# Optimization experiments

Hardware: AMD Instinct MI355X
Metric: run time of the kernel (lower is better)

Reference implementation:

```python
import jax, jax.numpy as jnp
import numpy as np

N = 50000          # nodes
E = 1_600_000      # edges (avg degree 32)
D = 128            # in_channels
H = 128            # hidden_channels
B = 4096           # batch_nodes
BETA = 0.5


def setup_inputs() -> dict:
    key = jax.random.key(0)
    ks = jax.random.split(key, 12)
    s = 1.0 / np.sqrt(D)
    inp = {
        "x": jax.random.normal(ks[0], (N, D), jnp.float32),
        "edge_index": jax.random.randint(ks[1], (2, E), 0, N, dtype=jnp.int64),
        "batch_nodes": jax.random.randint(ks[2], (B,), 0, N, dtype=jnp.int64),
        "labels": jax.random.randint(ks[3], (N,), 0, 2, dtype=jnp.int64),
        # GCNConv layer params (weight [in,out], bias [out])
        "W1": jax.random.uniform(ks[4], (D, H), jnp.float32, -s, s),
        "b1": jnp.zeros((H,), jnp.float32),
        "W2": jax.random.uniform(ks[5], (H, H), jnp.float32, -s, s),
        "b2": jnp.zeros((H,), jnp.float32),
        # Bilinear heads: weight [H,H] (out_features=1), scalar bias
        "W_ctx": jax.random.uniform(ks[6], (H, H), jnp.float32, -s, s),
        "b_ctx": jnp.zeros((), jnp.float32),
        "W_loc": jax.random.uniform(ks[7], (H, H), jnp.float32, -s, s),
        "b_loc": jnp.zeros((), jnp.float32),
    }
    return inp


def _gcn_conv(h, W, b, src, dst, n):
    """PyG GCNConv: linear transform, add self-loops, sym-normalized scatter-add."""
    h = h @ W  # [n, out]
    loop = jnp.arange(n, dtype=src.dtype)
    src_f = jnp.concatenate([src, loop])
    dst_f = jnp.concatenate([dst, loop])
    deg = jax.ops.segment_sum(jnp.ones_like(dst_f, dtype=h.dtype), dst_f, num_segments=n)
    dinv = jnp.where(deg > 0, jax.lax.rsqrt(deg), 0.0)
    norm = dinv[src_f] * dinv[dst_f]                      # [E+n]
    msg = h[src_f] * norm[:, None]                        # gather + scale
    out = jax.ops.segment_sum(msg, dst_f, num_segments=n)  # scatter-add
    return out + b


def _bce_logits(z, y):
    # mean(softplus(z) - z*y) == BCEWithLogits
    return jnp.mean(jax.nn.softplus(z) - z * y)


def reference(x, edge_index, batch_nodes, labels, W1, b1, W2, b2, W_ctx, b_ctx, W_loc, b_loc):
    src, dst = edge_index[0], edge_index[1]
    n = x.shape[0]
    layers = [(W1, b1), (W2, b2)]

    # eval mode: dropout is identity
    h = x
    for W, b in layers:
        h = jax.nn.relu(_gcn_conv(h, W, b, src, dst, n))

    gf = h[batch_nodes]                                   # [B, H]
    y = (labels[batch_nodes] == 1).astype(gf.dtype)       # [B]
    pos_cnt = jnp.sum(y)
    neg_cnt = y.shape[0] - pos_cnt
    pos_proto = (y[:, None] * gf).sum(0) / pos_cnt        # [H]

    # context bilinear head: z_i = gf_i^T W_ctx pos_proto + b (neg_sim is dead code in source)
    pos_sim = gf @ (W_ctx @ pos_proto) + b_ctx            # [B]
    ctx_loss = _bce_logits(pos_sim, y)

    # environment view: zero out batch nodes, re-run GCN stack (no dropout in source)
    masked_x = x.at[batch_nodes].set(0.0)
    env_h = masked_x
    for W, b in layers:
        env_h = jax.nn.relu(_gcn_conv(env_h, W, b, src, dst, n))
    env_f = env_h[batch_nodes]                            # [B, H]

    local_sim = jnp.einsum('nd,de,ne->n', env_f, W_loc, gf) + b_loc
    local_loss = _bce_logits(local_sim, 1.0 - y)

    total_loss = BETA * ctx_loss + (1.0 - BETA) * local_loss
    # source's guard: both classes present (true w.h.p. for random labels)
    total_loss = jnp.where((pos_cnt > 0) & (neg_cnt > 0), total_loss, 0.0)
    return gf, total_loss
```

## Files before the change

### kernel.cpp

```cpp
#include <hip/hip_runtime.h>
#include <math.h>

#define HID 128
#define BSH 7
#define BNODES 128
#define CAP 6144
#define NBK 512
#define EPB 4096

typedef _Float16 h2v __attribute__((ext_vector_type(2)));
typedef _Float16 h8v __attribute__((ext_vector_type(8)));
typedef float f4v __attribute__((ext_vector_type(4)));

static inline int ceil_div(int a, int b) { return (a + b - 1) / b; }


__global__ __launch_bounds__(256) void k_setup(const float* __restrict__ W1, const float* __restrict__ W2,
                                               const float* __restrict__ Wl, _Float16* T1, _Float16* T2,
                                               _Float16* Tl, unsigned int* mask, int* bcur,
                                               float* part, float* pcnt_raw, float* lsums, int* donecnt,
                                               int mw, int NB) {
    int b = blockIdx.x;
    int t = threadIdx.x;
    if (b < 192) {
        int which = b >> 6;
        int idx = (b & 63) * 256 + t;
        int k = idx >> 7, c = idx & 127;
        const float* S = (which == 0) ? W1 : ((which == 1) ? W2 : Wl);
        _Float16* D = (which == 0) ? T1 : ((which == 1) ? T2 : Tl);
        D[c * 128 + k] = (_Float16)S[idx];
    } else {
        int i = (b - 192) * 256 + t;
        if (i < mw) mask[i] = 0u;
        if (i < NB) bcur[i] = i * CAP;
        if (b == 192) {
            if (t < 128) part[t] = 0.f;
            else if (t == 128) pcnt_raw[0] = 0.f;
            else if (t < 131) lsums[t - 129] = 0.f;
            else if (t == 131) donecnt[0] = 0;
        }
    }
}


__global__ __launch_bounds__(1024) void k_partA(const int* __restrict__ ei, int* __restrict__ bcur,
                                                unsigned int* __restrict__ ebuf,
                                                const int* __restrict__ batch, unsigned int* mask,
                                                int E, int B, int NB, int NBLKE) {
    if ((int)blockIdx.x >= NBLKE) {
        int i = ((int)blockIdx.x - NBLKE) * 1024 + threadIdx.x;
        if (i < B) { int nd = batch[i]; atomicOr(&mask[nd >> 5], 1u << (nd & 31)); }
        return;
    }
    __shared__ int lcnt[NBK];
    __shared__ int sc[NBK];
    __shared__ int lcur[NBK];
    __shared__ int gbase[NBK];
    __shared__ unsigned int se[EPB];
    int tid = threadIdx.x;
    if (tid < NBK) lcnt[tid] = 0;
    __syncthreads();
    int base = blockIdx.x * EPB;
    unsigned int pk[4];
    int bk[4];
#pragma unroll
    for (int j = 0; j < 4; ++j) {
        int e = base + tid + j * 1024;
        if (e < E) {
            int s = ei[e], d = ei[E + e];
            pk[j] = ((unsigned int)s << 8) | (unsigned int)(d & 127);
            bk[j] = d >> BSH;
            atomicAdd(&lcnt[bk[j]], 1);
        } else bk[j] = -1;
    }
    __syncthreads();
    if (tid < NBK) sc[tid] = lcnt[tid];
    __syncthreads();
    for (int off = 1; off < NBK; off <<= 1) {
        int v = 0;
        if (tid < NBK && tid >= off) v = sc[tid - off];
        __syncthreads();
        if (tid < NBK) sc[tid] += v;
        __syncthreads();
    }
    if (tid < NBK) {
        int cc = lcnt[tid];
        lcur[tid] = sc[tid] - cc;
        gbase[tid] = cc ? atomicAdd(&bcur[tid], cc) : 0;
    }
    __syncthreads();
#pragma unroll
    for (int j = 0; j < 4; ++j) {
        if (bk[j] >= 0) {
            int r = atomicAdd(&lcur[bk[j]], 1);
            se[r] = pk[j];
        }
    }
    __syncthreads();
    int wid = tid >> 6, lane = tid & 63;
    for (int b2 = wid; b2 < NB; b2 += 16) {
        int cc = lcnt[b2];
        int lo = sc[b2] - cc;
        int go = gbase[b2];
        for (int i = lane; i < cc; i += 64) ebuf[go + i] = se[lo + i];
    }
}


__global__ __launch_bounds__(256) void k_csr(const unsigned int* __restrict__ ebuf, const int* __restrict__ bcur,
                                             const unsigned int* __restrict__ mask,
                                             float* __restrict__ sdinv, int* __restrict__ rs,
                                             int* __restrict__ degpk, unsigned int* __restrict__ csr, int N) {
    __shared__ unsigned int se[CAP];
    __shared__ int deg[BNODES];
    __shared__ int fde[BNODES];
    __shared__ int sc[BNODES];
    __shared__ int cu[BNODES];
    __shared__ int cf[BNODES];
    int b = blockIdx.x, t = threadIdx.x;
    if (t < BNODES) { deg[t] = 0; fde[t] = 0; }
    __syncthreads();
    int base = b * CAP;
    int ecnt = bcur[b] - base;
    for (int i = t; i < ecnt; i += 256) {
        unsigned int v = ebuf[base + i];
        int s = v >> 8;
        int fl = (mask[s >> 5] >> (s & 31)) & 1;
        se[i] = ((unsigned int)s << 9) | ((unsigned int)fl << 8) | (v & 255);
        atomicAdd(&deg[v & 255], 1);
        if (fl) atomicAdd(&fde[v & 255], 1);
    }
    __syncthreads();
    int dv = 0, fv = 0, pv = 0;
    if (t < BNODES) {
        dv = deg[t]; fv = fde[t];
        pv = (dv + 7) & ~7;
        sc[t] = pv;
    }
    __syncthreads();
    for (int off = 1; off < BNODES; off <<= 1) {
        int v2 = (t < BNODES && t >= off) ? sc[t - off] : 0;
        __syncthreads();
        if (t < BNODES) sc[t] += v2;
        __syncthreads();
    }
    int node = b * BNODES + t;
    int r0 = 0;
    if (t < BNODES) {
        r0 = base + sc[t] - pv;
        cu[t] = r0;
        cf[t] = r0 + (dv - fv);
        if (node < N) {
            rs[node] = r0;
            degpk[node] = dv | (fv << 16);
            float di = rsqrtf((float)(dv + 1));
            if ((mask[node >> 5] >> (node & 31)) & 1) di = -di;
            sdinv[node] = di;
        }
    }
    __syncthreads();
    for (int i = t; i < ecnt; i += 256) {
        unsigned int v = se[i];
        int d8 = v & 255;
        int p = ((v >> 8) & 1) ? atomicAdd(&cf[d8], 1) : atomicAdd(&cu[d8], 1);
        csr[p] = v >> 9;
    }
    if (t < BNODES && node < N) {
        for (int j = dv; j < pv; ++j) csr[r0 + j] = (unsigned int)N;
    }
}


__global__ __launch_bounds__(256) void k_cast(const float* __restrict__ x, const float* __restrict__ sdinv,
                                              _Float16* __restrict__ xs, _Float16* __restrict__ H, int N) {
    int i = blockIdx.x * 256 + threadIdx.x;
    int nx = N * 16;
    if (i < nx) {
        int node = i >> 4;
        float da = fabsf(sdinv[node]);
        int o = i * 8;
        float4 a = *(const float4*)&x[o];
        float4 b = *(const float4*)&x[o + 4];
        h8v v;
        v[0] = (_Float16)(a.x * da); v[1] = (_Float16)(a.y * da);
        v[2] = (_Float16)(a.z * da); v[3] = (_Float16)(a.w * da);
        v[4] = (_Float16)(b.x * da); v[5] = (_Float16)(b.y * da);
        v[6] = (_Float16)(b.z * da); v[7] = (_Float16)(b.w * da);
        *(h8v*)&xs[o] = v;
    } else if (i < nx + 16) {
        *(h8v*)&xs[(size_t)i * 8] = (h8v){};
    } else if (i < nx + 16 + 32) {
        int j = i - (nx + 16);
        *(h8v*)&H[(size_t)2 * N * HID + j * 8] = (h8v){};
    }
}


__global__ __launch_bounds__(512) void k_layer1(const _Float16* __restrict__ xs, const int* __restrict__ rs,
                                                const int* __restrict__ degpk, const unsigned int* __restrict__ csr,
                                                const float* __restrict__ sdinv, const _Float16* __restrict__ W1T,
                                                const float* __restrict__ bias, _Float16* __restrict__ H, int N) {
    __shared__ __align__(16) _Float16 sWT[128 * 136];
    __shared__ __align__(16) _Float16 sAgg[64 * 136];
    __shared__ float sbias[128];
    __shared__ float sda[32];
    float* sC = (float*)sWT;

    int tid = threadIdx.x;
    int wave = tid >> 6, lane = tid & 63;
    int grp = lane >> 4, rl = lane & 15;

#pragma unroll
    for (int it = 0; it < 4; ++it) {
        int lin = (it * 512 + tid) * 8;
        int c = lin >> 7, k = lin & 127;
        *(h8v*)&sWT[c * 136 + k] = *(const h8v*)&W1T[lin];
    }
    if (tid < 128) sbias[tid] = bias[tid];
    if (tid < 32) {
        int nd = blockIdx.x * 32 + tid;
        sda[tid] = (nd < N) ? fabsf(sdinv[nd]) : 0.f;
    }

    int ch = rl * 8;
    int lg = wave * 4 + grp;
    int row = blockIdx.x * 32 + lg;
    bool ok = row < N;
    int p = 0, deg = 0, fd = 0;
    float sd = 0.f;
    h8v hs = {};
    if (ok) {
        p = rs[row];
        int dp = degpk[row];
        deg = dp & 0xffff; fd = dp >> 16;
        sd = sdinv[row];
        hs = *(const h8v*)&xs[(size_t)row * HID + ch];
    }
    int ud = deg - fd;
    int pd = (deg + 7) & ~7;
    int t1 = max(pd, __shfl_xor(pd, 16));
    int m  = max(t1, __shfl_xor(t1, 32));
    float U[8] = {}, F[8] = {};
    for (int i = 0; i < m; i += 16) {
        int id[16];
#pragma unroll
        for (int k = 0; k < 16; ++k) {
            int raw = (int)csr[p + i + k];
            id[k] = (i + k < pd) ? raw : N;
        }
        h8v h[16];
#pragma unroll
        for (int k = 0; k < 16; ++k) h[k] = *(const h8v*)&xs[(size_t)id[k] * HID + ch];
        h8v s0 = (h[0] + h[1]) + (h[2] + h[3]);
        h8v s1 = (h[4] + h[5]) + (h[6] + h[7]);
        h8v s2 = (h[8] + h[9]) + (h[10] + h[11]);
        h8v s3 = (h[12] + h[13]) + (h[14] + h[15]);
        h8v s  = (s0 + s1) + (s2 + s3);
#pragma unroll
        for (int j = 0; j < 8; ++j) U[j] += (float)s[j];
        if (i + 16 > ud) {
#pragma unroll
            for (int k = 0; k < 16; ++k) {
                if (i + k >= ud && i + k < deg) {
#pragma unroll
                    for (int j = 0; j < 8; ++j) F[j] += (float)h[k][j];
                }
            }
        }
    }
    {
        float da = fabsf(sd);
        float keep = (sd < 0.f) ? 0.f : 1.f;
        h8v lo = {}, hi = {};
        if (ok) {
#pragma unroll
            for (int j = 0; j < 8; ++j) {
                float f = (float)hs[j];
                lo[j] = (_Float16)(da * (U[j] + f));
                hi[j] = (_Float16)(da * (U[j] - F[j] + keep * f));
            }
        }
        *(h8v*)&sAgg[(2 * lg) * 136 + ch] = lo;
        *(h8v*)&sAgg[(2 * lg + 1) * 136 + ch] = hi;
    }
    __syncthreads();

    int g = lane >> 4;
    int rowtile = (wave & 3) * 16;
    int colbase = (wave >> 2) * 64;
    f4v acc[4];
#pragma unroll
    for (int cc = 0; cc < 4; ++cc) acc[cc] = (f4v){0.f, 0.f, 0.f, 0.f};
#pragma unroll
    for (int kb = 0; kb < 4; ++kb) {
        int k0 = kb * 32 + g * 8;
        h8v av = *(const h8v*)&sAgg[(rowtile + rl) * 136 + k0];
#pragma unroll
        for (int cc = 0; cc < 4; ++cc) {
            h8v bv = *(const h8v*)&sWT[(colbase + cc * 16 + rl) * 136 + k0];
            acc[cc] = __builtin_amdgcn_mfma_f32_16x16x32_f16(bv, av, acc[cc], 0, 0, 0);
        }
    }
    __syncthreads();

    int lrow = rowtile + rl;
    float dsc = sda[lrow >> 1];
#pragma unroll
    for (int cc = 0; cc < 4; ++cc) {
        f4v v = acc[cc];
        int col = colbase + cc * 16 + g * 4;
#pragma unroll
        for (int i2 = 0; i2 < 4; ++i2) v[i2] = fmaxf(v[i2] + sbias[col + i2], 0.f) * dsc;
        *(f4v*)&sC[lrow * 132 + col] = v;
    }
    __syncthreads();

    int sr = tid >> 3, ck = tid & 7;
    int gRow = blockIdx.x * 64 + sr;
    if (gRow < 2 * N) {
        const float* src = &sC[sr * 132 + ck * 16];
        h8v o0, o1;
#pragma unroll
        for (int j = 0; j < 8; ++j) { o0[j] = (_Float16)src[j]; o1[j] = (_Float16)src[8 + j]; }
        _Float16* dst = &H[(size_t)gRow * HID + ck * 16];
        *(h8v*)&dst[0] = o0;
        *(h8v*)&dst[8] = o1;
    }
}


__global__ __launch_bounds__(512) void k_layer2(const _Float16* __restrict__ H, const int* __restrict__ rs,
                                                const int* __restrict__ degpk, const unsigned int* __restrict__ csr,
                                                const float* __restrict__ sdinv, const int* __restrict__ batch,
                                                const int* __restrict__ labels,
                                                const _Float16* __restrict__ W2T, const float* __restrict__ bias,
                                                float* __restrict__ gf, _Float16* __restrict__ envh,
                                                float* __restrict__ yv, float* __restrict__ part,
                                                float* __restrict__ pcnt_raw, int B, int N) {
    __shared__ __align__(16) _Float16 sWT[128 * 136];
    __shared__ __align__(16) _Float16 sAgg[32 * 136];
    __shared__ float sbias[128];
    __shared__ float sy2[16];
    float* sC = (float*)sWT;

    int tid = threadIdx.x;
    int wave = tid >> 6, lane = tid & 63;

#pragma unroll
    for (int it = 0; it < 4; ++it) {
        int lin = (it * 512 + tid) * 8;
        int c = lin >> 7, k = lin & 127;
        *(h8v*)&sWT[c * 136 + k] = *(const h8v*)&W2T[lin];
    }
    if (tid < 128) sbias[tid] = bias[tid];

    int rl32 = lane & 31;
    int view = rl32 >> 4;
    int rl = rl32 & 15;
    int ch = rl * 8;
    int lg = wave * 2 + (lane >> 5);
    int ri = blockIdx.x * 16 + lg;
    bool ok = ri < B;
    int p = 0, deg = 0, row = 0;
    float da = 0.f;
    h8v hsv = {};
    if (ok) {
        row = batch[ri];
        p = rs[row];
        deg = degpk[row] & 0xffff;
        da = fabsf(sdinv[row]);
        hsv = *(const h8v*)&H[(size_t)row * 256 + view * 128 + ch];
    }
    int pd = (deg + 7) & ~7;
    int m = max(pd, __shfl_xor(pd, 32));
    float a[8] = {};
    for (int i = 0; i < m; i += 8) {
        int id[8];
#pragma unroll
        for (int k = 0; k < 8; ++k) {
            int raw = (int)csr[p + i + k];
            id[k] = (i + k < pd) ? raw : N;
        }
        h8v x[8];
#pragma unroll
        for (int k = 0; k < 8; ++k) x[k] = *(const h8v*)&H[(size_t)id[k] * 256 + view * 128 + ch];
        h8v s = ((x[0] + x[1]) + (x[2] + x[3])) + ((x[4] + x[5]) + (x[6] + x[7]));
#pragma unroll
        for (int j = 0; j < 8; ++j) a[j] += (float)s[j];
    }
    {
        h8v lo = {};
        if (ok) {
#pragma unroll
            for (int j = 0; j < 8; ++j) lo[j] = (_Float16)(da * (a[j] + (float)hsv[j]));
        }
        *(h8v*)&sAgg[(2 * lg + view) * 136 + ch] = lo;
    }
    __syncthreads();

    int g = lane >> 4;
    int rl2 = lane & 15;
    int rowtile = (wave & 1) * 16;
    int colbase = (wave >> 1) * 32;
    f4v acc[2];
    acc[0] = (f4v){0.f, 0.f, 0.f, 0.f};
    acc[1] = (f4v){0.f, 0.f, 0.f, 0.f};
#pragma unroll
    for (int kb = 0; kb < 4; ++kb) {
        int k0 = kb * 32 + g * 8;
        h8v av = *(const h8v*)&sAgg[(rowtile + rl2) * 136 + k0];
#pragma unroll
        for (int cc = 0; cc < 2; ++cc) {
            h8v bv = *(const h8v*)&sWT[(colbase + cc * 16 + rl2) * 136 + k0];
            acc[cc] = __builtin_amdgcn_mfma_f32_16x16x32_f16(bv, av, acc[cc], 0, 0, 0);
        }
    }
    __syncthreads();

    int lrow = rowtile + rl2;
#pragma unroll
    for (int cc = 0; cc < 2; ++cc) {
        f4v v = acc[cc];
        int col = colbase + cc * 16 + g * 4;
#pragma unroll
        for (int i2 = 0; i2 < 4; ++i2) v[i2] = fmaxf(v[i2] + sbias[col + i2], 0.f);
        *(f4v*)&sC[lrow * 132 + col] = v;
    }
    __syncthreads();

    int sr = tid >> 4, ck = tid & 15;
    int ri2 = blockIdx.x * 16 + (sr >> 1);
    if (ri2 < B) {
        const float* src = &sC[sr * 132 + ck * 8];
        if ((sr & 1) == 0) {
            float* dst = &gf[(size_t)ri2 * HID + ck * 8];
            *(float4*)&dst[0] = *(const float4*)&src[0];
            *(float4*)&dst[4] = *(const float4*)&src[4];
        } else {
            h8v o;
#pragma unroll
            for (int j = 0; j < 8; ++j) o[j] = (_Float16)src[j];
            *(h8v*)&envh[(size_t)ri2 * HID + ck * 8] = o;
        }
    }

    int rr = blockIdx.x * 16 + tid;
    if (tid < 16) {
        float y = 0.f;
        if (rr < B) {
            y = (labels[batch[rr]] == 1) ? 1.f : 0.f;
            yv[rr] = y;
        }
        sy2[tid] = y;
    }
    __syncthreads();
    if (tid < 128) {
        float acc2 = 0.f;
#pragma unroll
        for (int r2 = 0; r2 < 16; ++r2) acc2 += sy2[r2] * sC[(2 * r2) * 132 + tid];
        atomicAdd(&part[tid], acc2);
    } else if (tid == 128) {
        float ps = 0.f;
#pragma unroll
        for (int r2 = 0; r2 < 16; ++r2) ps += sy2[r2];
        atomicAdd(&pcnt_raw[0], ps);
    }
}


__global__ __launch_bounds__(256) void k_headsT(const _Float16* __restrict__ envh, const float* __restrict__ gf,
                                                const _Float16* __restrict__ WlT, const float* __restrict__ Wctx,
                                                const float* __restrict__ part, const float* __restrict__ pcnt_raw,
                                                const float* __restrict__ yv, const float* __restrict__ bctx,
                                                const float* __restrict__ bloc, float* __restrict__ lsums,
                                                int* __restrict__ donecnt, float* __restrict__ out_loss,
                                                int B, int nblk) {
    __shared__ __align__(16) _Float16 sWT[128 * 136];
    __shared__ float sv[128];
    __shared__ float sproto[128];
    int tid = threadIdx.x;
#pragma unroll
    for (int it = 0; it < 8; ++it) {
        int lin = (it * 256 + tid) * 8;
        int c = lin >> 7, k = lin & 127;
        *(h8v*)&sWT[c * 136 + k] = *(const h8v*)&WlT[lin];
    }
    if (tid < 128) sproto[tid] = part[tid] / pcnt_raw[0];
    __syncthreads();
    if (tid < 128) {
        float acc = 0.f;
#pragma unroll 4
        for (int j = 0; j < 128; ++j) acc += Wctx[tid * 128 + j] * sproto[j];
        sv[tid] = acc;
    }
    __syncthreads();

    int wave = tid >> 6, lane = tid & 63;
    int rl = lane & 15, g = lane >> 4;
    int r = blockIdx.x * 64 + wave * 16 + rl;
    bool rok = r < B;
    f4v acc[8];
#pragma unroll
    for (int cf = 0; cf < 8; ++cf) acc[cf] = (f4v){0.f, 0.f, 0.f, 0.f};
#pragma unroll
    for (int kb = 0; kb < 4; ++kb) {
        int k0 = kb * 32 + g * 8;
        h8v av = {};
        if (rok) av = *(const h8v*)&envh[(size_t)r * HID + k0];
#pragma unroll
        for (int cf = 0; cf < 8; ++cf) {
            h8v bv = *(const h8v*)&sWT[(cf * 16 + rl) * 136 + k0];
            acc[cf] = __builtin_amdgcn_mfma_f32_16x16x32_f16(bv, av, acc[cf], 0, 0, 0);
        }
    }
    float s1 = 0.f, s2 = 0.f;
    if (rok) {
#pragma unroll
        for (int cf = 0; cf < 8; ++cf) {
            int col = cf * 16 + g * 4;
            float4 gv = *(const float4*)&gf[(size_t)r * HID + col];
            s2 += acc[cf][0] * gv.x + acc[cf][1] * gv.y + acc[cf][2] * gv.z + acc[cf][3] * gv.w;
            s1 += sv[col] * gv.x + sv[col + 1] * gv.y + sv[col + 2] * gv.z + sv[col + 3] * gv.w;
        }
    }
    s1 += __shfl_xor(s1, 16); s1 += __shfl_xor(s1, 32);
    s2 += __shfl_xor(s2, 16); s2 += __shfl_xor(s2, 32);
    float l1 = 0.f, l2 = 0.f;
    if (g == 0 && rok) {
        float y = yv[r];
        float z1 = s1 + bctx[0];
        float z2 = s2 + bloc[0];
        l1 = fmaxf(z1, 0.f) + log1pf(expf(-fabsf(z1))) - z1 * y;
        l2 = fmaxf(z2, 0.f) + log1pf(expf(-fabsf(z2))) - z2 * (1.f - y);
    }
#pragma unroll
    for (int o = 1; o < 64; o <<= 1) {
        l1 += __shfl_xor(l1, o);
        l2 += __shfl_xor(l2, o);
    }
    if (lane == 0) {
        atomicAdd(&lsums[0], l1);
        atomicAdd(&lsums[1], l2);
    }
    __syncthreads();
    if (tid == 0) {
        __threadfence();
        int old = atomicAdd(donecnt, 1);
        if (old == nblk - 1) {
            float l1s = atomicAdd(&lsums[0], 0.f);
            float l2s = atomicAdd(&lsums[1], 0.f);
            float pc = pcnt_raw[0];
            float nc = (float)B - pc;
            float total = 0.5f * (l1s / (float)B) + 0.5f * (l2s / (float)B);
            out_loss[0] = (pc > 0.f && nc > 0.f) ? total : 0.f;
        }
    }
}


extern "C" void kernel_launch(void* const* d_in, const int* in_sizes, int n_in,
                              void* d_out, int out_size, void* d_ws, size_t ws_size,
                              hipStream_t stream) {
    const float* x      = (const float*)d_in[0];
    const int*   ei     = (const int*)d_in[1];
    const int*   batch  = (const int*)d_in[2];
    const int*   labels = (const int*)d_in[3];
    const float* W1     = (const float*)d_in[4];
    const float* b1     = (const float*)d_in[5];
    const float* W2     = (const float*)d_in[6];
    const float* b2     = (const float*)d_in[7];
    const float* Wctx   = (const float*)d_in[8];
    const float* bctx   = (const float*)d_in[9];
    const float* Wloc   = (const float*)d_in[10];
    const float* bloc   = (const float*)d_in[11];

    int N = in_sizes[0] / HID;
    int E = in_sizes[1] / 2;
    int B = in_sizes[2];
    float* out = (float*)d_out;

    char* wsb = (char*)d_ws;
    size_t off = 0;
    auto alloc = [&](size_t bytes) -> char* {
        char* p = wsb + off;
        off += (bytes + 255) & ~(size_t)255;
        return p;
    };
    int NB = ceil_div(N, BNODES);
    int mw = ceil_div(N, 32);

    _Float16* xs   = (_Float16*)alloc((size_t)(N + 1) * HID * 2);
    _Float16* H    = (_Float16*)alloc((size_t)(2 * N + 2) * HID * 2);
    unsigned int* ebuf = (unsigned int*)alloc((size_t)NB * CAP * 4);
    unsigned int* csr  = (unsigned int*)alloc((size_t)NB * CAP * 4);
    float* sdinv = (float*)alloc((size_t)N * 4);
    int*   rs    = (int*)alloc((size_t)N * 4);
    int*   degpk = (int*)alloc((size_t)N * 4);
    int*   bcur  = (int*)alloc((size_t)NB * 4);
    unsigned int* mask = (unsigned int*)alloc((size_t)mw * 4);
    _Float16* W1T = (_Float16*)alloc(128 * 128 * 2);
    _Float16* W2T = (_Float16*)alloc(128 * 128 * 2);
    _Float16* WlT = (_Float16*)alloc(128 * 128 * 2);
    _Float16* envh  = (_Float16*)alloc((size_t)B * HID * 2);
    float* yv    = (float*)alloc((size_t)B * 4);
    float* part  = (float*)alloc(128 * 4);
    float* pcnt_raw = (float*)alloc(256);
    float* lsums = (float*)alloc(256);
    int*   donecnt = (int*)alloc(256);
    (void)ws_size; (void)n_in; (void)out_size;

    int NBLKE = ceil_div(E, EPB);
    int NBLKB = ceil_div(B, 1024);
    int NHB = ceil_div(B, 64);

    k_setup<<<192 + ceil_div(mw, 256), 256, 0, stream>>>(W1, W2, Wloc, W1T, W2T, WlT, mask, bcur,
                                                         part, pcnt_raw, lsums, donecnt, mw, NB);
    k_partA<<<NBLKE + NBLKB, 1024, 0, stream>>>(ei, bcur, ebuf, batch, mask, E, B, NB, NBLKE);
    k_csr<<<NB, 256, 0, stream>>>(ebuf, bcur, mask, sdinv, rs, degpk, csr, N);
    k_cast<<<ceil_div(N * 16 + 48, 256), 256, 0, stream>>>(x, sdinv, xs, H, N);

    k_layer1<<<ceil_div(N, 32), 512, 0, stream>>>(xs, rs, degpk, csr, sdinv, W1T, b1, H, N);

    k_layer2<<<ceil_div(B, 16), 512, 0, stream>>>(H, rs, degpk, csr, sdinv, batch, labels, W2T, b2,
                                                  out, envh, yv, part, pcnt_raw, B, N);

    k_headsT<<<NHB, 256, 0, stream>>>(envh, out, WlT, Wctx, part, pcnt_raw, yv, bctx, bloc,
                                      lsums, donecnt, out + (size_t)B * HID, B, NHB);
}
```

Before: 145.5 us.

## Split layer-1 into channel-quarter gather passes plus a separate MFMA GEMM

Replaces the fused gather+GEMM layer-1 kernel with four gather launches, each aggregating a 32-channel quarter of neighbour features into an intermediate buffer, followed by a standalone MFMA GEMM kernel. Working on one channel quarter per pass shrinks the per-pass gather footprint so the x table slice fits better in cache, and it removes the per-wave max-degree padding. The cost is an extra round trip through global memory for the 2N×128 aggregated buffer and more kernel launches.

```diff
diff --git a/kernel.cpp b/kernel.cpp
--- a/kernel.cpp
+++ b/kernel.cpp
@@ -196,35 +196,14 @@
 }
 
 
-__global__ __launch_bounds__(512) void k_layer1(const _Float16* __restrict__ xs, const int* __restrict__ rs,
+__global__ __launch_bounds__(256) void k_gather(const _Float16* __restrict__ xs, const int* __restrict__ rs,
                                                 const int* __restrict__ degpk, const unsigned int* __restrict__ csr,
-                                                const float* __restrict__ sdinv, const _Float16* __restrict__ W1T,
-                                                const float* __restrict__ bias, _Float16* __restrict__ H, int N) {
-    __shared__ __align__(16) _Float16 sWT[128 * 136];
-    __shared__ __align__(16) _Float16 sAgg[64 * 136];
-    __shared__ float sbias[128];
-    __shared__ float sda[32];
-    float* sC = (float*)sWT;
-
+                                                const float* __restrict__ sdinv, _Float16* __restrict__ aggX,
+                                                int q, int N) {
     int tid = threadIdx.x;
-    int wave = tid >> 6, lane = tid & 63;
-    int grp = lane >> 4, rl = lane & 15;
-
-#pragma unroll
-    for (int it = 0; it < 4; ++it) {
-        int lin = (it * 512 + tid) * 8;
-        int c = lin >> 7, k = lin & 127;
-        *(h8v*)&sWT[c * 136 + k] = *(const h8v*)&W1T[lin];
-    }
-    if (tid < 128) sbias[tid] = bias[tid];
-    if (tid < 32) {
-        int nd = blockIdx.x * 32 + tid;
-        sda[tid] = (nd < N) ? fabsf(sdinv[nd]) : 0.f;
-    }
-
-    int ch = rl * 8;
-    int lg = wave * 4 + grp;
-    int row = blockIdx.x * 32 + lg;
+    int row = blockIdx.x * 64 + (tid >> 2);
+    int lane2 = tid & 3;
+    int ch = q * 32 + lane2 * 8;
     bool ok = row < N;
     int p = 0, deg = 0, fd = 0;
     float sd = 0.f;
@@ -238,10 +217,8 @@
     }
     int ud = deg - fd;
     int pd = (deg + 7) & ~7;
-    int t1 = max(pd, __shfl_xor(pd, 16));
-    int m  = max(t1, __shfl_xor(t1, 32));
     float U[8] = {}, F[8] = {};
-    for (int i = 0; i < m; i += 16) {
+    for (int i = 0; i < pd; i += 16) {
         int id[16];
 #pragma unroll
         for (int k = 0; k < 16; ++k) {
@@ -268,63 +245,80 @@
             }
         }
     }
-    {
-        float da = fabsf(sd);
-        float keep = (sd < 0.f) ? 0.f : 1.f;
-        h8v lo = {}, hi = {};
-        if (ok) {
-#pragma unroll
-            for (int j = 0; j < 8; ++j) {
-                float f = (float)hs[j];
-                lo[j] = (_Float16)(da * (U[j] + f));
-                hi[j] = (_Float16)(da * (U[j] - F[j] + keep * f));
-            }
-        }
-        *(h8v*)&sAgg[(2 * lg) * 136 + ch] = lo;
-        *(h8v*)&sAgg[(2 * lg + 1) * 136 + ch] = hi;
-    }
-    __syncthreads();
-
-    int g = lane >> 4;
-    int rowtile = (wave & 3) * 16;
-    int colbase = (wave >> 2) * 64;
-    f4v acc[4];
-#pragma unroll
-    for (int cc = 0; cc < 4; ++cc) acc[cc] = (f4v){0.f, 0.f, 0.f, 0.f};
+    if (!ok) return;
+    float da = fabsf(sd);
+    float keep = (sd < 0.f) ? 0.f : 1.f;
+    h8v lo, hi;
+#pragma unroll
+    for (int j = 0; j < 8; ++j) {
+        float f = (float)hs[j];
+        lo[j] = (_Float16)(da * (U[j] + f));
+        hi[j] = (_Float16)(da * (U[j] - F[j] + keep * f));
+    }
+    *(h8v*)&aggX[(size_t)row * 256 + ch] = lo;
+    *(h8v*)&aggX[(size_t)row * 256 + 128 + ch] = hi;
+}
+
+
+__global__ __launch_bounds__(256) void k_gemm1(const _Float16* __restrict__ A, const _Float16* __restrict__ WT,
+                                               const float* __restrict__ bias, const float* __restrict__ sdinv,
+                                               _Float16* __restrict__ outH, int n2) {
+    __shared__ __align__(16) char smem[128 * 136 * 2];
+    __shared__ float sbias[128];
+    _Float16* sWT = (_Float16*)smem;
+    float* sC = (float*)smem;
+    int tid = threadIdx.x;
+#pragma unroll
+    for (int it = 0; it < 8; ++it) {
+        int lin = (it * 256 + tid) * 8;
+        int c = lin >> 7, k = lin & 127;
+        *(h8v*)&sWT[c * 136 + k] = *(const h8v*)&WT[lin];
+    }
+    if (tid < 128) sbias[tid] = bias[tid];
+    __syncthreads();
+
+    int wave = tid >> 6, lane = tid & 63;
+    int rl = lane & 15, g = lane >> 4;
+    int r = blockIdx.x * 64 + wave * 16 + rl;
+    bool rok = r < n2;
+    f4v acc[8];
+#pragma unroll
+    for (int cf = 0; cf < 8; ++cf) acc[cf] = (f4v){0.f, 0.f, 0.f, 0.f};
 #pragma unroll
     for (int kb = 0; kb < 4; ++kb) {
         int k0 = kb * 32 + g * 8;
-        h8v av = *(const h8v*)&sAgg[(rowtile + rl) * 136 + k0];
-#pragma unroll
-        for (int cc = 0; cc < 4; ++cc) {
-            h8v bv = *(const h8v*)&sWT[(colbase + cc * 16 + rl) * 136 + k0];
-            acc[cc] = __builtin_amdgcn_mfma_f32_16x16x32_f16(bv, av, acc[cc], 0, 0, 0);
-        }
-    }
-    __syncthreads();
-
-    int lrow = rowtile + rl;
-    float dsc = sda[lrow >> 1];
-#pragma unroll
-    for (int cc = 0; cc < 4; ++cc) {
-        f4v v = acc[cc];
-        int col = colbase + cc * 16 + g * 4;
-#pragma unroll
-        for (int i2 = 0; i2 < 4; ++i2) v[i2] = fmaxf(v[i2] + sbias[col + i2], 0.f) * dsc;
-        *(f4v*)&sC[lrow * 132 + col] = v;
-    }
-    __syncthreads();
-
-    int sr = tid >> 3, ck = tid & 7;
-    int gRow = blockIdx.x * 64 + sr;
-    if (gRow < 2 * N) {
-        const float* src = &sC[sr * 132 + ck * 16];
-        h8v o0, o1;
-#pragma unroll
-        for (int j = 0; j < 8; ++j) { o0[j] = (_Float16)src[j]; o1[j] = (_Float16)src[8 + j]; }
-        _Float16* dst = &H[(size_t)gRow * HID + ck * 16];
-        *(h8v*)&dst[0] = o0;
-        *(h8v*)&dst[8] = o1;
+        h8v av = {};
+        if (rok) av = *(const h8v*)&A[(size_t)r * HID + k0];
+#pragma unroll
+        for (int cf = 0; cf < 8; ++cf) {
+            h8v bv = *(const h8v*)&sWT[(cf * 16 + rl) * 136 + k0];
+            acc[cf] = __builtin_amdgcn_mfma_f32_16x16x32_f16(bv, av, acc[cf], 0, 0, 0);
+        }
+    }
+    __syncthreads();
+    int lrow = wave * 16 + rl;
+#pragma unroll
+    for (int cf = 0; cf < 8; ++cf) {
+        f4v v = acc[cf];
+        int chh = cf * 16 + g * 4;
+#pragma unroll
+        for (int i2 = 0; i2 < 4; ++i2) v[i2] = fmaxf(v[i2] + sbias[chh + i2], 0.f);
+        *(f4v*)&sC[lrow * 132 + cf * 16 + g * 4] = v;
+    }
+    __syncthreads();
+    int lr = tid >> 2, seg = tid & 3;
+    int R = blockIdx.x * 64 + lr;
+    if (R < n2) {
+        const float* src = &sC[lr * 132 + seg * 32];
+        float scale = fabsf(sdinv[R >> 1]);
+        _Float16* dst = &outH[(size_t)R * HID + seg * 32];
+#pragma unroll
+        for (int qq = 0; qq < 4; ++qq) {
+            h8v o;
+#pragma unroll
+            for (int j = 0; j < 8; ++j) o[j] = (_Float16)(src[qq * 8 + j] * scale);
+            *(h8v*)&dst[qq * 8] = o;
+        }
     }
 }
 
@@ -590,6 +584,7 @@
     int mw = ceil_div(N, 32);
 
     _Float16* xs   = (_Float16*)alloc((size_t)(N + 1) * HID * 2);
+    _Float16* aggX = (_Float16*)alloc((size_t)N * 256 * 2);
     _Float16* H    = (_Float16*)alloc((size_t)(2 * N + 2) * HID * 2);
     unsigned int* ebuf = (unsigned int*)alloc((size_t)NB * CAP * 4);
     unsigned int* csr  = (unsigned int*)alloc((size_t)NB * CAP * 4);
@@ -619,7 +614,12 @@
     k_csr<<<NB, 256, 0, stream>>>(ebuf, bcur, mask, sdinv, rs, degpk, csr, N);
     k_cast<<<ceil_div(N * 16 + 48, 256), 256, 0, stream>>>(x, sdinv, xs, H, N);
 
-    k_layer1<<<ceil_div(N, 32), 512, 0, stream>>>(xs, rs, degpk, csr, sdinv, W1T, b1, H, N);
+    int NGB = ceil_div(N, 64);
+    k_gather<<<NGB, 256, 0, stream>>>(xs, rs, degpk, csr, sdinv, aggX, 0, N);
+    k_gather<<<NGB, 256, 0, stream>>>(xs, rs, degpk, csr, sdinv, aggX, 1, N);
+    k_gather<<<NGB, 256, 0, stream>>>(xs, rs, degpk, csr, sdinv, aggX, 2, N);
+    k_gather<<<NGB, 256, 0, stream>>>(xs, rs, degpk, csr, sdinv, aggX, 3, N);
+    k_gemm1<<<ceil_div(2 * N, 64), 256, 0, stream>>>(aggX, W1T, b1, sdinv, H, 2 * N);
 
     k_layer2<<<ceil_div(B, 16), 512, 0, stream>>>(H, rs, degpk, csr, sdinv, batch, labels, W2T, b2,
                                                   out, envh, yv, part, pcnt_raw, B, N);
```

After: 196.8 us. 35.2% more time.
